# Performance work log

Hardware: AMD Instinct MI355X
Metric: run time of the kernel (lower is better)

The kernel has to match this reference:

```python
import math
import jax, jax.numpy as jnp
import numpy as np

D_MODEL = 1024
HEADS = 16
D_K = D_MODEL // HEADS
BATCH = 4
SEQ = 2048


def setup_inputs() -> dict:
    key = jax.random.key(0)
    ks = jax.random.split(key, 7)
    q = jax.random.normal(ks[0], (BATCH, SEQ, D_MODEL), dtype=jnp.float32)
    k = jax.random.normal(ks[1], (BATCH, SEQ, D_MODEL), dtype=jnp.float32)
    v = jax.random.normal(ks[2], (BATCH, SEQ, D_MODEL), dtype=jnp.float32)
    # causal mask: True = masked (filled with -inf), broadcastable over batch & heads
    mask = jnp.triu(jnp.ones((SEQ, SEQ), dtype=bool), k=1)[None, None, :, :]
    s = 1.0 / math.sqrt(D_MODEL)
    Wq = jax.random.normal(ks[3], (D_MODEL, D_MODEL), dtype=jnp.float32) * s
    Wk = jax.random.normal(ks[4], (D_MODEL, D_MODEL), dtype=jnp.float32) * s
    Wv = jax.random.normal(ks[5], (D_MODEL, D_MODEL), dtype=jnp.float32) * s
    Wo = jax.random.normal(ks[6], (D_MODEL, D_MODEL), dtype=jnp.float32) * s
    return {"q": q, "k": k, "v": v, "mask": mask, "Wq": Wq, "Wk": Wk, "Wv": Wv, "Wo": Wo}


def reference(q, k, v, mask, Wq, Wk, Wv, Wo):
    B, S, _ = q.shape
    # Linear(d_model, d_model, bias=False): y = x @ W.T
    def proj(x, W):
        return (x @ W.T).reshape(B, S, HEADS, D_K).transpose(0, 2, 1, 3)  # [B,H,S,Dk]
    qh, kh, vh = proj(q, Wq), proj(k, Wk), proj(v, Wv)
    scores = jnp.einsum('bhqd,bhkd->bhqk', qh, kh) / math.sqrt(D_K)
    scores = jnp.where(mask, -jnp.inf, scores)
    attn = jax.nn.softmax(scores, axis=-1)  # dropout p=0 is identity
    ctx = jnp.einsum('bhqk,bhkd->bhqd', attn, vh)
    ctx = ctx.transpose(0, 2, 1, 3).reshape(B, S, D_MODEL)
    return ctx @ Wo.T
```

## Files before the change

kernel.cpp:

```cpp
#include <hip/hip_runtime.h>
#include <hip/hip_bf16.h>
#include <stdint.h>

#define S_LEN 2048
#define DMODEL 1024
#define HEADS 16
#define DK 64
#define LDK 72

#define QSCALE 0.18033688011112042f

typedef __attribute__((ext_vector_type(8))) short bf16x8;
typedef __attribute__((ext_vector_type(4))) float f32x4;

__device__ __forceinline__ unsigned short f2bf(float f) {
    union { float f; unsigned u; } c; c.f = f;
    unsigned u = c.u;
    u += 0x7fffu + ((u >> 16) & 1u);
    return (unsigned short)(u >> 16);
}

__device__ __forceinline__ unsigned pkbf(float a, float b) {
    union { float f; unsigned u; } ca, cb; ca.f = a; cb.f = b;
    unsigned ua = ca.u + (0x7fffu + ((ca.u >> 16) & 1u));
    unsigned ub = cb.u + (0x7fffu + ((cb.u >> 16) & 1u));
    return __builtin_amdgcn_perm(ub, ua, 0x07060302);
}

__device__ __forceinline__ unsigned cvtpk(float a, float b) {
    unsigned r;
    asm("v_cvt_pk_bf16_f32 %0, %1, %2" : "=v"(r) : "v"(a), "v"(b));
    return r;
}

__device__ __forceinline__ void g2lds16(const unsigned short* g, unsigned short* l) {
    __builtin_amdgcn_global_load_lds((const __attribute__((address_space(1))) void*)g,
                                     (__attribute__((address_space(3))) void*)l, 16, 0, 0);
}

__global__ __launch_bounds__(256) void convert_kernel(
    const float* __restrict__ q, const float* __restrict__ k, const float* __restrict__ v,
    const float* __restrict__ Wq, const float* __restrict__ Wk, const float* __restrict__ Wv,
    const float* __restrict__ Wo,
    unsigned short* __restrict__ qbf, unsigned short* __restrict__ kbf,
    unsigned short* __restrict__ vbf, unsigned short* __restrict__ wbf)
{
    const float* src; unsigned short* dst; int n8;
    const int y = blockIdx.y;
    if (y == 0)      { src = q;  dst = qbf;           n8 = 1048576; }
    else if (y == 1) { src = k;  dst = kbf;           n8 = 1048576; }
    else if (y == 2) { src = v;  dst = vbf;           n8 = 1048576; }
    else if (y == 3) { src = Wq; dst = wbf;           n8 = 131072; }
    else if (y == 4) { src = Wk; dst = wbf + 1048576; n8 = 131072; }
    else if (y == 5) { src = Wv; dst = wbf + 2097152; n8 = 131072; }
    else             { src = Wo; dst = wbf + 3145728; n8 = 131072; }
    int i = blockIdx.x * 256 + threadIdx.x;
    if (i >= n8) return;
    float4 f0 = ((const float4*)src)[(size_t)2 * i];
    float4 f1 = ((const float4*)src)[(size_t)2 * i + 1];
    union { unsigned u[4]; uint4 v; } o;
    o.u[0] = pkbf(f0.x, f0.y); o.u[1] = pkbf(f0.z, f0.w);
    o.u[2] = pkbf(f1.x, f1.y); o.u[3] = pkbf(f1.z, f1.w);
    *(uint4*)&dst[(size_t)8 * i] = o.v;
}

__device__ __forceinline__ void gemm_core_256x128(
    const unsigned short* __restrict__ Apanel,
    const unsigned short* __restrict__ Bpanel,
    unsigned short* sm,
    f32x4 acc[4][4])
{
    const int t    = threadIdx.x;
    const int lane = t & 63;
    const int w    = t >> 6;
    const int wm   = w >> 1;
    const int wn   = w & 1;
    const int lrow = lane & 15;
    const int quad = lane >> 4;

    const int l8   = lane >> 3;
    const int c16s = (lane & 7) ^ l8;
    const unsigned short* gA = Apanel + (size_t)(w * 8 + l8) * 1024 + c16s * 8;
    const unsigned short* gB = Bpanel + (size_t)(w * 8 + l8) * 1024 + c16s * 8;
    unsigned short* lA = sm + w * 512;
    unsigned short* lB = sm + 16384 + w * 512;

#define STAGE_KT(bufsel, kt) do {                                         \
        unsigned short* la = lA + (bufsel) * 24576;                       \
        unsigned short* lb = lB + (bufsel) * 24576;                       \
        const unsigned short* ga = gA + (kt) * 64;                        \
        const unsigned short* gb = gB + (kt) * 64;                        \
        g2lds16(ga,                        la);                           \
        g2lds16(ga + (size_t) 64 * 1024,   la + 4096);                    \
        g2lds16(ga + (size_t)128 * 1024,   la + 8192);                    \
        g2lds16(ga + (size_t)192 * 1024,   la + 12288);                   \
        g2lds16(gb,                        lb);                           \
        g2lds16(gb + (size_t) 64 * 1024,   lb + 4096);                    \
    } while (0)

    for (int i = 0; i < 4; i++) for (int j = 0; j < 4; j++) acc[i][j] = (f32x4){0.f, 0.f, 0.f, 0.f};

    STAGE_KT(0, 0);

#pragma unroll 1
    for (int kt = 0; kt < 16; ++kt) {
        const int buf = kt & 1;
        if (kt < 15) {
            STAGE_KT(buf ^ 1, kt + 1);
            asm volatile("s_waitcnt vmcnt(6)" ::: "memory");
        } else {
            asm volatile("s_waitcnt vmcnt(0)" ::: "memory");
        }
        __builtin_amdgcn_sched_barrier(0);
        __builtin_amdgcn_s_barrier();
        __builtin_amdgcn_sched_barrier(0);

        const unsigned short* tA = sm + buf * 24576;
        const unsigned short* tB = sm + buf * 24576 + 16384;
        for (int kh = 0; kh < 2; ++kh) {
            const int cs = ((kh * 4 + quad) ^ (lrow & 7)) * 8;
            bf16x8 a[4], b[4];
            for (int mi = 0; mi < 4; mi++)
                a[mi] = *(const bf16x8*)&tA[(wm * 64 + mi * 16 + lrow) * 64 + cs];
            for (int nj = 0; nj < 4; nj++)
                b[nj] = *(const bf16x8*)&tB[(wn * 64 + nj * 16 + lrow) * 64 + cs];
            __builtin_amdgcn_s_setprio(1);
            for (int mi = 0; mi < 4; mi++)
                for (int nj = 0; nj < 4; nj++)
                    acc[mi][nj] = __builtin_amdgcn_mfma_f32_16x16x32_bf16(a[mi], b[nj], acc[mi][nj], 0, 0, 0);
            __builtin_amdgcn_s_setprio(0);
        }
        __builtin_amdgcn_sched_barrier(0);
        __builtin_amdgcn_s_barrier();
        __builtin_amdgcn_sched_barrier(0);
    }
#undef STAGE_KT
}

__global__ __launch_bounds__(512, 2) void proj_gemm_kernel(
    const unsigned short* __restrict__ qbf, const unsigned short* __restrict__ kbf,
    const unsigned short* __restrict__ vbf, const unsigned short* __restrict__ wbf,
    unsigned short* __restrict__ qh, unsigned short* __restrict__ kh,
    unsigned short* __restrict__ vh_t)
{
    const unsigned short* A; const unsigned short* Bm; unsigned short* Y;
    const int z = blockIdx.z;
    if (z == 0)      { A = qbf; Bm = wbf;           Y = qh;   }
    else if (z == 1) { A = kbf; Bm = wbf + 1048576; Y = kh;   }
    else             { A = vbf; Bm = wbf + 2097152; Y = vh_t; }

    __shared__ unsigned short sm[49152];

    const int m0 = blockIdx.x * 256;
    const int n0 = blockIdx.y * 128;

    f32x4 acc[4][4];
    gemm_core_256x128(A + (size_t)m0 * 1024, Bm + (size_t)n0 * 1024, sm, acc);

    const int t = threadIdx.x, lane = t & 63;
    const int wm = (t >> 6) >> 1, wn = (t >> 6) & 1;
    const int lrow = lane & 15, quad = lane >> 4;
    const float scale = (z == 0) ? QSCALE : 1.0f;
    for (int i = 0; i < 4; i++) {
        int grow = m0 + wm * 64 + i * 16 + quad * 4;
        for (int j = 0; j < 4; j++) {
            int gcol = n0 + wn * 64 + j * 16 + lrow;
            int h = gcol >> 6, d = gcol & 63;
            for (int r = 0; r < 4; r++) {
                int row = grow + r;
                int b_ = row >> 11;
                int s_ = row & 2047;
                unsigned short val = f2bf(acc[i][j][r] * scale);
                if (z == 2)
                    Y[(((size_t)(b_ * HEADS + h) * DK) + d) * S_LEN + s_] = val;
                else
                    Y[(((size_t)(b_ * HEADS + h) * S_LEN) + s_) * DK + d] = val;
            }
        }
    }
}

__global__ __launch_bounds__(512, 2) void outproj_gemm_kernel(
    const unsigned short* __restrict__ ctx, const unsigned short* __restrict__ wobf,
    float* __restrict__ out)
{
    __shared__ unsigned short sm[49152];

    const int m0 = blockIdx.x * 256;
    const int n0 = blockIdx.y * 128;

    f32x4 acc[4][4];
    gemm_core_256x128(ctx + (size_t)m0 * 1024, wobf + (size_t)n0 * 1024, sm, acc);

    const int t = threadIdx.x, lane = t & 63;
    const int wm = (t >> 6) >> 1, wn = (t >> 6) & 1;
    const int lrow = lane & 15, quad = lane >> 4;
    for (int i = 0; i < 4; i++) {
        int grow = m0 + wm * 64 + i * 16 + quad * 4;
        for (int j = 0; j < 4; j++) {
            int gcol = n0 + wn * 64 + j * 16 + lrow;
            for (int r = 0; r < 4; r++)
                out[(size_t)(grow + r) * DMODEL + gcol] = acc[i][j][r];
        }
    }
}

__global__ __launch_bounds__(256, 4) void attn_kernel(
    const unsigned short* __restrict__ qh, const unsigned short* __restrict__ kh,
    const unsigned short* __restrict__ vh_t, unsigned short* __restrict__ ctx)
{
    __shared__ unsigned short sK[64 * LDK];
    __shared__ unsigned short sVt[64 * LDK];
    __shared__ unsigned short sPT[4][16 * LDK];

    const int t    = threadIdx.x;
    const int lane = t & 63;
    const int wid  = t >> 6;
    const int lin  = (int)(blockIdx.y * gridDim.x + blockIdx.x);
    const int wlin = (lin & 7) * 128 + (lin >> 3);
    const int qx   = wlin & 15;
    const int bh   = wlin >> 4;
    const size_t base = (size_t)bh * S_LEN * DK;
    const int lrow = lane & 15;
    const int quad = lane >> 4;
    const int b_ = bh >> 4, h_ = bh & 15;
    unsigned short* myPT = &sPT[wid][0];

    const int sr0 = t >> 3;
    const int sc0 = (t & 7) * 8;
    const unsigned short* gK = kh + base;
    const unsigned short* gV = vh_t + base;

    for (int pass = 0; pass < 2; ++pass) {
        const int qt = pass ? (31 - qx) : qx;
        const int q0 = qt * 64;
        const int qw0 = q0 + wid * 16;

        bf16x8 qreg[2];
        for (int h = 0; h < 2; ++h)
            qreg[h] = *(const bf16x8*)&qh[base + (size_t)(qw0 + lrow) * DK + h * 32 + quad * 8];

        f32x4 o[4];
        for (int mf = 0; mf < 4; mf++) o[mf] = (f32x4){0.f, 0.f, 0.f, 0.f};
        float lstat = 0.f;

        const int ntiles = qt + 1;

        uint4 rK0 = *(const uint4*)&gK[(size_t)sr0 * DK + sc0];
        uint4 rK1 = *(const uint4*)&gK[(size_t)(sr0 + 32) * DK + sc0];
        uint4 rV0 = *(const uint4*)&gV[(size_t)sr0 * S_LEN + sc0];
        uint4 rV1 = *(const uint4*)&gV[(size_t)(sr0 + 32) * S_LEN + sc0];

        for (int kt = 0; kt < ntiles; ++kt) {
            const int k0 = kt * 64;
            __syncthreads();
            *(uint4*)&sK [sr0 * LDK + sc0]        = rK0;
            *(uint4*)&sK [(sr0 + 32) * LDK + sc0] = rK1;
            *(uint4*)&sVt[sr0 * LDK + sc0]        = rV0;
            *(uint4*)&sVt[(sr0 + 32) * LDK + sc0] = rV1;
            if (kt + 1 < ntiles) {
                const int kn = k0 + 64;
                rK0 = *(const uint4*)&gK[(size_t)(kn + sr0) * DK + sc0];
                rK1 = *(const uint4*)&gK[(size_t)(kn + sr0 + 32) * DK + sc0];
                rV0 = *(const uint4*)&gV[(size_t)sr0 * S_LEN + kn + sc0];
                rV1 = *(const uint4*)&gV[(size_t)(sr0 + 32) * S_LEN + kn + sc0];
            }
            __syncthreads();

            f32x4 st[4];
            for (int mf = 0; mf < 4; mf++) st[mf] = (f32x4){0.f, 0.f, 0.f, 0.f};
            for (int h = 0; h < 2; ++h) {
                bf16x8 kf[4];
                for (int mf = 0; mf < 4; mf++)
                    kf[mf] = *(const bf16x8*)&sK[(mf * 16 + lrow) * LDK + h * 32 + quad * 8];
                __builtin_amdgcn_s_setprio(1);
                for (int mf = 0; mf < 4; mf++)
                    st[mf] = __builtin_amdgcn_mfma_f32_16x16x32_bf16(kf[mf], qreg[h], st[mf], 0, 0, 0);
                __builtin_amdgcn_s_setprio(0);
            }

            if (kt == qt) {
                const int qidx = qw0 + lrow;
                for (int mf = 0; mf < 4; mf++)
                    for (int r = 0; r < 4; r++) {
                        int key = k0 + mf * 16 + quad * 4 + r;
                        if (key > qidx) st[mf][r] = -INFINITY;
                    }
            }

            {
                float rsum = 0.f;
                for (int mf = 0; mf < 4; mf++) {
                    float p0 = exp2f(st[mf][0]);
                    float p1 = exp2f(st[mf][1]);
                    float p2 = exp2f(st[mf][2]);
                    float p3 = exp2f(st[mf][3]);
                    rsum += (p0 + p1) + (p2 + p3);
                    uint2 pk;
                    pk.x = cvtpk(p0, p1);
                    pk.y = cvtpk(p2, p3);
                    *(uint2*)&myPT[lrow * LDK + mf * 16 + quad * 4] = pk;
                }
                lstat += rsum;
            }

            for (int h = 0; h < 2; ++h) {
                bf16x8 vf[4];
                for (int mf = 0; mf < 4; mf++)
                    vf[mf] = *(const bf16x8*)&sVt[(mf * 16 + lrow) * LDK + h * 32 + quad * 8];
                bf16x8 pf = *(const bf16x8*)&myPT[lrow * LDK + h * 32 + quad * 8];
                __builtin_amdgcn_s_setprio(1);
                for (int mf = 0; mf < 4; mf++)
                    o[mf] = __builtin_amdgcn_mfma_f32_16x16x32_bf16(vf[mf], pf, o[mf], 0, 0, 0);
                __builtin_amdgcn_s_setprio(0);
            }
        }

        {
            float ls = lstat;
            ls += __shfl_xor(ls, 16);
            ls += __shfl_xor(ls, 32);
            float inv = 1.f / ls;
            int s_ = qw0 + lrow;
            size_t rowbase = (((size_t)(b_ * S_LEN + s_)) * HEADS + h_) * DK;
            for (int mf = 0; mf < 4; mf++) {
                int d0 = mf * 16 + quad * 4;
                uint2 pk;
                pk.x = pkbf(o[mf][0] * inv, o[mf][1] * inv);
                pk.y = pkbf(o[mf][2] * inv, o[mf][3] * inv);
                *(uint2*)&ctx[rowbase + d0] = pk;
            }
        }
    }
}

__global__ __launch_bounds__(256) void proj_fb_kernel(
    const float* __restrict__ q, const float* __restrict__ k, const float* __restrict__ v,
    const float* __restrict__ Wq, const float* __restrict__ Wk, const float* __restrict__ Wv,
    unsigned short* __restrict__ qh, unsigned short* __restrict__ kh, unsigned short* __restrict__ vh_t)
{
    const float* X; const float* W; unsigned short* Y;
    if (blockIdx.z == 0)      { X = q; W = Wq; Y = qh; }
    else if (blockIdx.z == 1) { X = k; W = Wk; Y = kh; }
    else                      { X = v; W = Wv; Y = vh_t; }

    __shared__ short sA[128 * LDK];
    __shared__ short sB[128 * LDK];
    const int t = threadIdx.x, lane = t & 63, wid = t >> 6;
    const int wrow = (wid >> 1) * 64, wcol = (wid & 1) * 64;
    const int m0 = blockIdx.x * 128, n0 = blockIdx.y * 128;
    const int lrow = lane & 15, quad = lane >> 4, lk = quad * 8;

    f32x4 acc[4][4];
    for (int i = 0; i < 4; i++) for (int j = 0; j < 4; j++) acc[i][j] = (f32x4){0.f, 0.f, 0.f, 0.f};

    for (int kb = 0; kb < DMODEL; kb += 64) {
        for (int it = 0; it < 8; ++it) {
            int idx = t + it * 256;
            int row = idx >> 4, c4 = (idx & 15) * 4;
            float4 fa = *(const float4*)&X[(size_t)(m0 + row) * DMODEL + kb + c4];
            float4 fb = *(const float4*)&W[(size_t)(n0 + row) * DMODEL + kb + c4];
            short4 sa = { (short)f2bf(fa.x), (short)f2bf(fa.y), (short)f2bf(fa.z), (short)f2bf(fa.w) };
            short4 sb = { (short)f2bf(fb.x), (short)f2bf(fb.y), (short)f2bf(fb.z), (short)f2bf(fb.w) };
            *(short4*)&sA[row * LDK + c4] = sa;
            *(short4*)&sB[row * LDK + c4] = sb;
        }
        __syncthreads();
        for (int kk = 0; kk < 64; kk += 32) {
            bf16x8 a[4], b[4];
            for (int i = 0; i < 4; i++) a[i] = *(const bf16x8*)&sA[(wrow + i * 16 + lrow) * LDK + kk + lk];
            for (int j = 0; j < 4; j++) b[j] = *(const bf16x8*)&sB[(wcol + j * 16 + lrow) * LDK + kk + lk];
            for (int i = 0; i < 4; i++)
                for (int j = 0; j < 4; j++)
                    acc[i][j] = __builtin_amdgcn_mfma_f32_16x16x32_bf16(a[i], b[j], acc[i][j], 0, 0, 0);
        }
        __syncthreads();
    }

    const float scale = (blockIdx.z == 0) ? QSCALE : 1.0f;
    for (int i = 0; i < 4; i++) {
        int grow = m0 + wrow + i * 16 + quad * 4;
        for (int j = 0; j < 4; j++) {
            int gcol = n0 + wcol + j * 16 + lrow;
            int h = gcol >> 6, d = gcol & 63;
            for (int r = 0; r < 4; r++) {
                int row = grow + r, b_ = row >> 11, s_ = row & 2047;
                unsigned short val = f2bf(acc[i][j][r] * scale);
                if (blockIdx.z == 2)
                    Y[(((size_t)(b_ * HEADS + h) * DK) + d) * S_LEN + s_] = val;
                else
                    Y[(((size_t)(b_ * HEADS + h) * S_LEN) + s_) * DK + d] = val;
            }
        }
    }
}

__global__ __launch_bounds__(256) void outproj_fb_kernel(
    const unsigned short* __restrict__ ctx, const float* __restrict__ Wo, float* __restrict__ out)
{
    __shared__ short sA[128 * LDK];
    __shared__ short sB[128 * LDK];
    const int t = threadIdx.x, lane = t & 63, wid = t >> 6;
    const int wrow = (wid >> 1) * 64, wcol = (wid & 1) * 64;
    const int m0 = blockIdx.x * 128, n0 = blockIdx.y * 128;
    const int lrow = lane & 15, quad = lane >> 4, lk = quad * 8;

    f32x4 acc[4][4];
    for (int i = 0; i < 4; i++) for (int j = 0; j < 4; j++) acc[i][j] = (f32x4){0.f, 0.f, 0.f, 0.f};

    for (int kb = 0; kb < DMODEL; kb += 64) {
        for (int it = 0; it < 4; ++it) {
            int idx = t + it * 256;
            int row = idx >> 3, c8 = (idx & 7) * 8;
            *(uint4*)&sA[row * LDK + c8] = *(const uint4*)&ctx[(size_t)(m0 + row) * DMODEL + kb + c8];
        }
        for (int it = 0; it < 8; ++it) {
            int idx = t + it * 256;
            int row = idx >> 4, c4 = (idx & 15) * 4;
            float4 fb = *(const float4*)&Wo[(size_t)(n0 + row) * DMODEL + kb + c4];
            short4 sb = { (short)f2bf(fb.x), (short)f2bf(fb.y), (short)f2bf(fb.z), (short)f2bf(fb.w) };
            *(short4*)&sB[row * LDK + c4] = sb;
        }
        __syncthreads();
        for (int kk = 0; kk < 64; kk += 32) {
            bf16x8 a[4], b[4];
            for (int i = 0; i < 4; i++) a[i] = *(const bf16x8*)&sA[(wrow + i * 16 + lrow) * LDK + kk + lk];
            for (int j = 0; j < 4; j++) b[j] = *(const bf16x8*)&sB[(wcol + j * 16 + lrow) * LDK + kk + lk];
            for (int i = 0; i < 4; i++)
                for (int j = 0; j < 4; j++)
                    acc[i][j] = __builtin_amdgcn_mfma_f32_16x16x32_bf16(a[i], b[j], acc[i][j], 0, 0, 0);
        }
        __syncthreads();
    }

    for (int i = 0; i < 4; i++) {
        int grow = m0 + wrow + i * 16 + quad * 4;
        for (int j = 0; j < 4; j++) {
            int gcol = n0 + wcol + j * 16 + lrow;
            for (int r = 0; r < 4; r++)
                out[(size_t)(grow + r) * DMODEL + gcol] = acc[i][j][r];
        }
    }
}

extern "C" void kernel_launch(void* const* d_in, const int* in_sizes, int n_in,
                              void* d_out, int out_size, void* d_ws, size_t ws_size,
                              hipStream_t stream)
{
    const float* q  = (const float*)d_in[0];
    const float* k  = (const float*)d_in[1];
    const float* v  = (const float*)d_in[2];
    const float* Wq = (const float*)d_in[4];
    const float* Wk = (const float*)d_in[5];
    const float* Wv = (const float*)d_in[6];
    const float* Wo = (const float*)d_in[7];
    float* out = (float*)d_out;

    const size_t M8 = (size_t)8 * 1024 * 1024;
    const size_t need = (size_t)(52) * 1024 * 1024 * 2;

    if (ws_size >= need) {
        unsigned short* qbf  = (unsigned short*)d_ws;
        unsigned short* kbf  = qbf + M8;
        unsigned short* vbf  = kbf + M8;
        unsigned short* wbf  = vbf + M8;
        unsigned short* qh   = wbf + (size_t)4 * 1024 * 1024;
        unsigned short* kh   = qh + M8;
        unsigned short* vh_t = kh + M8;
        unsigned short* ctx  = qbf;

        dim3 gCvt(4096, 7);
        convert_kernel<<<gCvt, 256, 0, stream>>>(q, k, v, Wq, Wk, Wv, Wo, qbf, kbf, vbf, wbf);

        dim3 gProj(32, 8, 3);
        proj_gemm_kernel<<<gProj, 512, 0, stream>>>(qbf, kbf, vbf, wbf, qh, kh, vh_t);

        dim3 gAttn(16, 64);
        attn_kernel<<<gAttn, 256, 0, stream>>>(qh, kh, vh_t, ctx);

        dim3 gOut(32, 8);
        outproj_gemm_kernel<<<gOut, 512, 0, stream>>>(ctx, wbf + (size_t)3 * 1024 * 1024, out);
    } else {
        unsigned short* qh   = (unsigned short*)d_ws;
        unsigned short* kh   = qh + M8;
        unsigned short* vh_t = kh + M8;
        unsigned short* ctx  = vh_t + M8;

        dim3 gProj(64, 8, 3);
        proj_fb_kernel<<<gProj, 256, 0, stream>>>(q, k, v, Wq, Wk, Wv, qh, kh, vh_t);

        dim3 gAttn(16, 64);
        attn_kernel<<<gAttn, 256, 0, stream>>>(qh, kh, vh_t, ctx);

        dim3 gOut(64, 8);
        outproj_fb_kernel<<<gOut, 256, 0, stream>>>(ctx, Wo, out);
    }
}
```

Baseline: 327.8 us.

## Shrink projection GEMM tiles to 128x128 and remap blocks for XCD locality

The projection and output GEMMs move from 256x128 tiles with 512 threads to 128x128 tiles with 256 threads. That doubles the grid (1536 and 512 blocks) and cuts LDS per block, so more blocks fit per CU. Block indices are also remapped so that blocks sharing A panels land on the same XCD (the h&7 interleave), aiming for better L2 reuse. The cost is lower arithmetic intensity per tile and more total global loads of the A and B panels.

Result: no change. 329.0 us (+0.3%).

```diff
diff --git a/kernel.cpp b/kernel.cpp
--- a/kernel.cpp
+++ b/kernel.cpp
@@ -64,7 +64,7 @@
     *(uint4*)&dst[(size_t)8 * i] = o.v;
 }
 
-__device__ __forceinline__ void gemm_core_256x128(
+__device__ __forceinline__ void gemm_core_128x128(
     const unsigned short* __restrict__ Apanel,
     const unsigned short* __restrict__ Bpanel,
     unsigned short* sm,
@@ -83,19 +83,21 @@
     const unsigned short* gA = Apanel + (size_t)(w * 8 + l8) * 1024 + c16s * 8;
     const unsigned short* gB = Bpanel + (size_t)(w * 8 + l8) * 1024 + c16s * 8;
     unsigned short* lA = sm + w * 512;
-    unsigned short* lB = sm + 16384 + w * 512;
+    unsigned short* lB = sm + 8192 + w * 512;
 
 #define STAGE_KT(bufsel, kt) do {                                         \
-        unsigned short* la = lA + (bufsel) * 24576;                       \
-        unsigned short* lb = lB + (bufsel) * 24576;                       \
+        unsigned short* la = lA + (bufsel) * 16384;                       \
+        unsigned short* lb = lB + (bufsel) * 16384;                       \
         const unsigned short* ga = gA + (kt) * 64;                        \
         const unsigned short* gb = gB + (kt) * 64;                        \
-        g2lds16(ga,                        la);                           \
-        g2lds16(ga + (size_t) 64 * 1024,   la + 4096);                    \
-        g2lds16(ga + (size_t)128 * 1024,   la + 8192);                    \
-        g2lds16(ga + (size_t)192 * 1024,   la + 12288);                   \
-        g2lds16(gb,                        lb);                           \
-        g2lds16(gb + (size_t) 64 * 1024,   lb + 4096);                    \
+        g2lds16(ga,                       la);                            \
+        g2lds16(ga + (size_t)32 * 1024,   la + 2048);                     \
+        g2lds16(ga + (size_t)64 * 1024,   la + 4096);                     \
+        g2lds16(ga + (size_t)96 * 1024,   la + 6144);                     \
+        g2lds16(gb,                       lb);                            \
+        g2lds16(gb + (size_t)32 * 1024,   lb + 2048);                     \
+        g2lds16(gb + (size_t)64 * 1024,   lb + 4096);                     \
+        g2lds16(gb + (size_t)96 * 1024,   lb + 6144);                     \
     } while (0)
 
     for (int i = 0; i < 4; i++) for (int j = 0; j < 4; j++) acc[i][j] = (f32x4){0.f, 0.f, 0.f, 0.f};
@@ -107,7 +109,7 @@
         const int buf = kt & 1;
         if (kt < 15) {
             STAGE_KT(buf ^ 1, kt + 1);
-            asm volatile("s_waitcnt vmcnt(6)" ::: "memory");
+            asm volatile("s_waitcnt vmcnt(8)" ::: "memory");
         } else {
             asm volatile("s_waitcnt vmcnt(0)" ::: "memory");
         }
@@ -115,8 +117,8 @@
         __builtin_amdgcn_s_barrier();
         __builtin_amdgcn_sched_barrier(0);
 
-        const unsigned short* tA = sm + buf * 24576;
-        const unsigned short* tB = sm + buf * 24576 + 16384;
+        const unsigned short* tA = sm + buf * 16384;
+        const unsigned short* tB = sm + buf * 16384 + 8192;
         for (int kh = 0; kh < 2; ++kh) {
             const int cs = ((kh * 4 + quad) ^ (lrow & 7)) * 8;
             bf16x8 a[4], b[4];
@@ -137,25 +139,31 @@
 #undef STAGE_KT
 }
 
-__global__ __launch_bounds__(512, 2) void proj_gemm_kernel(
+__global__ __launch_bounds__(256, 2) void proj_gemm_kernel(
     const unsigned short* __restrict__ qbf, const unsigned short* __restrict__ kbf,
     const unsigned short* __restrict__ vbf, const unsigned short* __restrict__ wbf,
     unsigned short* __restrict__ qh, unsigned short* __restrict__ kh,
     unsigned short* __restrict__ vh_t)
 {
+    const int h   = (int)(blockIdx.x + 64 * (blockIdx.y + 8 * blockIdx.z));
+    const int s   = h >> 3;
+    const int panel = (h & 7) * 24 + (s >> 3);
+    const int by  = s & 7;
+    const int z   = panel >> 6;
+    const int bx  = panel & 63;
+
     const unsigned short* A; const unsigned short* Bm; unsigned short* Y;
-    const int z = blockIdx.z;
     if (z == 0)      { A = qbf; Bm = wbf;           Y = qh;   }
     else if (z == 1) { A = kbf; Bm = wbf + 1048576; Y = kh;   }
     else             { A = vbf; Bm = wbf + 2097152; Y = vh_t; }
 
-    __shared__ unsigned short sm[49152];
-
-    const int m0 = blockIdx.x * 256;
-    const int n0 = blockIdx.y * 128;
+    __shared__ unsigned short sm[32768];
+
+    const int m0 = bx * 128;
+    const int n0 = by * 128;
 
     f32x4 acc[4][4];
-    gemm_core_256x128(A + (size_t)m0 * 1024, Bm + (size_t)n0 * 1024, sm, acc);
+    gemm_core_128x128(A + (size_t)m0 * 1024, Bm + (size_t)n0 * 1024, sm, acc);
 
     const int t = threadIdx.x, lane = t & 63;
     const int wm = (t >> 6) >> 1, wn = (t >> 6) & 1;
@@ -165,32 +173,37 @@
         int grow = m0 + wm * 64 + i * 16 + quad * 4;
         for (int j = 0; j < 4; j++) {
             int gcol = n0 + wn * 64 + j * 16 + lrow;
-            int h = gcol >> 6, d = gcol & 63;
+            int hh = gcol >> 6, d = gcol & 63;
             for (int r = 0; r < 4; r++) {
                 int row = grow + r;
                 int b_ = row >> 11;
                 int s_ = row & 2047;
                 unsigned short val = f2bf(acc[i][j][r] * scale);
                 if (z == 2)
-                    Y[(((size_t)(b_ * HEADS + h) * DK) + d) * S_LEN + s_] = val;
+                    Y[(((size_t)(b_ * HEADS + hh) * DK) + d) * S_LEN + s_] = val;
                 else
-                    Y[(((size_t)(b_ * HEADS + h) * S_LEN) + s_) * DK + d] = val;
-            }
-        }
-    }
-}
-
-__global__ __launch_bounds__(512, 2) void outproj_gemm_kernel(
+                    Y[(((size_t)(b_ * HEADS + hh) * S_LEN) + s_) * DK + d] = val;
+            }
+        }
+    }
+}
+
+__global__ __launch_bounds__(256, 2) void outproj_gemm_kernel(
     const unsigned short* __restrict__ ctx, const unsigned short* __restrict__ wobf,
     float* __restrict__ out)
 {
-    __shared__ unsigned short sm[49152];
-
-    const int m0 = blockIdx.x * 256;
-    const int n0 = blockIdx.y * 128;
+    const int h   = (int)(blockIdx.x + 64 * blockIdx.y);
+    const int s   = h >> 3;
+    const int bx  = (h & 7) * 8 + (s >> 3);
+    const int by  = s & 7;
+
+    __shared__ unsigned short sm[32768];
+
+    const int m0 = bx * 128;
+    const int n0 = by * 128;
 
     f32x4 acc[4][4];
-    gemm_core_256x128(ctx + (size_t)m0 * 1024, wobf + (size_t)n0 * 1024, sm, acc);
+    gemm_core_128x128(ctx + (size_t)m0 * 1024, wobf + (size_t)n0 * 1024, sm, acc);
 
     const int t = threadIdx.x, lane = t & 63;
     const int wm = (t >> 6) >> 1, wn = (t >> 6) & 1;
@@ -472,14 +485,14 @@
         dim3 gCvt(4096, 7);
         convert_kernel<<<gCvt, 256, 0, stream>>>(q, k, v, Wq, Wk, Wv, Wo, qbf, kbf, vbf, wbf);
 
-        dim3 gProj(32, 8, 3);
-        proj_gemm_kernel<<<gProj, 512, 0, stream>>>(qbf, kbf, vbf, wbf, qh, kh, vh_t);
+        dim3 gProj(64, 8, 3);
+        proj_gemm_kernel<<<gProj, 256, 0, stream>>>(qbf, kbf, vbf, wbf, qh, kh, vh_t);
 
         dim3 gAttn(16, 64);
         attn_kernel<<<gAttn, 256, 0, stream>>>(qh, kh, vh_t, ctx);
 
-        dim3 gOut(32, 8);
-        outproj_gemm_kernel<<<gOut, 512, 0, stream>>>(ctx, wbf + (size_t)3 * 1024 * 1024, out);
+        dim3 gOut(64, 8);
+        outproj_gemm_kernel<<<gOut, 256, 0, stream>>>(ctx, wbf + (size_t)3 * 1024 * 1024, out);
     } else {
         unsigned short* qh   = (unsigned short*)d_ws;
         unsigned short* kh   = qh + M8;
```
